# Kernel optimization log

Hardware: AMD Instinct MI355X
Metric: run time of the kernel (lower is better)

Reference implementation:

```python
import jax, jax.numpy as jnp
import numpy as np

LOGIT_SCALE = 1.0 / 0.07  # from ClipLoss(temperature=0.07)


def setup_inputs() -> dict:
    key = jax.random.key(0)
    k1, k2 = jax.random.split(key)
    N, D = 16384, 512
    return {
        "image_features": jax.random.normal(k1, (N, D), dtype=jnp.float32),
        "text_features": jax.random.normal(k2, (N, D), dtype=jnp.float32),
    }


def reference(image_features, text_features):
    # logits_per_image[i, j] = scale * <img_i, txt_j>; logits_per_text is its transpose
    logits_per_image = LOGIT_SCALE * (image_features @ text_features.T)  # [N, N]
    logits_per_text = logits_per_image.T
    n = logits_per_image.shape[0]
    labels = jnp.arange(n)
    # cross_entropy(logits, labels) = mean over rows of (logsumexp(row) - row[label])
    def ce(logits):
        logp = jax.nn.log_softmax(logits, axis=-1)
        return -jnp.mean(jnp.take_along_axis(logp, labels[:, None], axis=-1))
    return (ce(logits_per_image) + ce(logits_per_text)) / 2.0
```

## Files before the change

### kernel.cpp

```cpp
#include <hip/hip_runtime.h>
#include <cstdint>
#include <cstddef>
#include <cmath>


#define N_ROWS 16384
#define DIM    512
#define NB     128
#define SCALE  14.285714285714286f
#define CF     20.609929155556625f
#define LN2F   0.6931471805599453f
#define SP     36

typedef __attribute__((ext_vector_type(8))) int   int8v;
typedef __attribute__((ext_vector_type(4))) int   int4v;
typedef __attribute__((ext_vector_type(4))) float floatx4;

#if __has_builtin(__builtin_amdgcn_exp2f)
#define EXP2(x) __builtin_amdgcn_exp2f(x)
#else
#define EXP2(x) exp2f(x)
#endif

__device__ __forceinline__ void async_load16(const void* g, void* l) {
    __builtin_amdgcn_global_load_lds(
        (__attribute__((address_space(1))) void*)(void*)(g),
        (__attribute__((address_space(3))) void*)(l), 16, 0, 0);
}

__device__ __forceinline__ void lse_merge2(float& m, float& s, float om, float os) {
    float nm = fmaxf(m, om);
    s = s * EXP2(m - nm) + os * EXP2(om - nm);
    m = nm;
}

__device__ __forceinline__ int pk_fp8x4(float a, float b, float c, float d) {
    int u = __builtin_amdgcn_cvt_pk_fp8_f32(a, b, 0, false);
    u = __builtin_amdgcn_cvt_pk_fp8_f32(c, d, u, true);
    return u;
}

__global__ void cvt_diag_kernel(const float* __restrict__ a, const float* __restrict__ b,
                                unsigned char* __restrict__ A8, unsigned char* __restrict__ B8,
                                float* __restrict__ diag) {
    const int t  = threadIdx.x;
    const int rl = t & 15, g16 = t >> 4;
    const int row = blockIdx.x * 16 + rl;
    const float4* ai = (const float4*)(a + (size_t)row * DIM + g16 * 32);
    const float4* bi = (const float4*)(b + (size_t)row * DIM + g16 * 32);
    float dot = 0.f;
    int wa[8], wb[8];
#pragma unroll
    for (int j = 0; j < 4; ++j) {
        float4 x0 = ai[2 * j], x1 = ai[2 * j + 1];
        float4 y0 = bi[2 * j], y1 = bi[2 * j + 1];
        dot += x0.x * y0.x + x0.y * y0.y + x0.z * y0.z + x0.w * y0.w
             + x1.x * y1.x + x1.y * y1.y + x1.z * y1.z + x1.w * y1.w;
        wa[2 * j]     = pk_fp8x4(CF * x0.x, CF * x0.y, CF * x0.z, CF * x0.w);
        wa[2 * j + 1] = pk_fp8x4(CF * x1.x, CF * x1.y, CF * x1.z, CF * x1.w);
        wb[2 * j]     = pk_fp8x4(y0.x, y0.y, y0.z, y0.w);
        wb[2 * j + 1] = pk_fp8x4(y1.x, y1.y, y1.z, y1.w);
    }
    const size_t o = ((size_t)g16 * N_ROWS + row) * 32;
    *(int4v*)(A8 + o)      = (int4v){wa[0], wa[1], wa[2], wa[3]};
    *(int4v*)(A8 + o + 16) = (int4v){wa[4], wa[5], wa[6], wa[7]};
    *(int4v*)(B8 + o)      = (int4v){wb[0], wb[1], wb[2], wb[3]};
    *(int4v*)(B8 + o + 16) = (int4v){wb[4], wb[5], wb[6], wb[7]};

    __shared__ float pd[16][17];
    pd[rl][g16] = dot;
    __syncthreads();
    if (t < 16) {
        float s = 0.f;
#pragma unroll
        for (int j = 0; j < 16; ++j) s += pd[t][j];
        diag[blockIdx.x * 16 + t] = SCALE * s;
    }
}

__global__ void gemm_lse_kernel(const unsigned char* __restrict__ A8,
                                const unsigned char* __restrict__ B8,
                                float* __restrict__ row_m, float* __restrict__ row_s,
                                float* __restrict__ col_m, float* __restrict__ col_s) {
    __shared__ __align__(16) unsigned char smem[32768];
    unsigned char* sA = smem;
    unsigned char* sB = smem + 16384;
    float* part = (float*)smem;

    const int t = threadIdx.x;
    const int bid = blockIdx.x;

    const int xcd   = bid & 7;
    const int local = bid >> 3;
    const int br    = xcd * 16 + (local & 15);
    const int bc    = local >> 4;

    const int lane = t & 63;
    const int w    = t >> 6;
    const int quad = lane >> 4;
    const int l15  = lane & 15;
    const int wrow = w >> 1;
    const int wcol = w & 1;

    floatx4 acc[4][4];
#pragma unroll
    for (int i = 0; i < 4; ++i)
#pragma unroll
        for (int j = 0; j < 4; ++j)
            acc[i][j] = (floatx4){0.f, 0.f, 0.f, 0.f};

    const int isB   = w >> 1;
    const int gbase = (w & 1) * 2;
    const unsigned char* gsrc = isB ? B8 : A8;
    const int rbase = (isB ? bc : br) * 128;
    unsigned char* lbase = isB ? sB : sA;

    const unsigned char* gp[8];
    unsigned char* lp[8];
#pragma unroll
    for (int c = 0; c < 8; ++c) {
        const int g = gbase + (c >> 2), i = c & 3;
        gp[c] = gsrc + ((size_t)g * N_ROWS + rbase) * 32 + i * 1024 + lane * 16;
        lp[c] = lbase + g * 4096 + i * 1024;
    }
    const size_t kbstr = (size_t)4 * N_ROWS * 32;

    for (int kb = 0; kb < 4; ++kb) {
        const size_t ko = (size_t)kb * kbstr;
#pragma unroll
        for (int c = 0; c < 8; ++c) async_load16(gp[c] + ko, lp[c]);
        __builtin_amdgcn_s_waitcnt(0);
        __syncthreads();

        int8v av[4], bv[4];
#pragma unroll
        for (int mi = 0; mi < 4; ++mi) {
            const unsigned char* p = sA + (quad * 128 + wrow * 64 + mi * 16 + l15) * 32;
            int4v lo = *(const int4v*)p;
            int4v hi = *(const int4v*)(p + 16);
            av[mi] = (int8v){lo[0], lo[1], lo[2], lo[3], hi[0], hi[1], hi[2], hi[3]};
        }
#pragma unroll
        for (int ni = 0; ni < 4; ++ni) {
            const unsigned char* p = sB + (quad * 128 + wcol * 64 + ni * 16 + l15) * 32;
            int4v lo = *(const int4v*)p;
            int4v hi = *(const int4v*)(p + 16);
            bv[ni] = (int8v){lo[0], lo[1], lo[2], lo[3], hi[0], hi[1], hi[2], hi[3]};
        }
#pragma unroll
        for (int mi = 0; mi < 4; ++mi)
#pragma unroll
            for (int ni = 0; ni < 4; ++ni)
                acc[mi][ni] = __builtin_amdgcn_mfma_scale_f32_16x16x128_f8f6f4(
                    av[mi], bv[ni], acc[mi][ni], 0, 0, 0, 127, 0, 127);
        __syncthreads();
    }


#pragma unroll
    for (int mi = 0; mi < 4; ++mi)
#pragma unroll
        for (int r = 0; r < 4; ++r) {
            float pm = fmaxf(fmaxf(acc[mi][0][r], acc[mi][1][r]),
                             fmaxf(acc[mi][2][r], acc[mi][3][r]));
            int lrow = wrow * 64 + mi * 16 + quad * 4 + r;
            part[lrow * SP + wcol * 16 + l15] = pm;
        }

#pragma unroll
    for (int ni = 0; ni < 4; ++ni) {
        float m = acc[0][ni][0];
#pragma unroll
        for (int mi = 0; mi < 4; ++mi)
#pragma unroll
            for (int r = 0; r < 4; ++r)
                m = fmaxf(m, acc[mi][ni][r]);
        m = fmaxf(m, __shfl_xor(m, 16));
        m = fmaxf(m, __shfl_xor(m, 32));
        float s = 0.f;
#pragma unroll
        for (int mi = 0; mi < 4; ++mi)
#pragma unroll
            for (int r = 0; r < 4; ++r)
                s += EXP2(acc[mi][ni][r] - m);
        s += __shfl_xor(s, 16);
        s += __shfl_xor(s, 32);
        if (quad == 0) {
            int cl = wcol * 64 + ni * 16 + l15;
            part[cl * SP + 32 + wrow] = m;
            part[cl * SP + 34 + wrow] = s;
        }
    }
    __syncthreads();

    if (t < 128) {
        float m = part[t * SP + 32], s = part[t * SP + 34];
        lse_merge2(m, s, part[t * SP + 33], part[t * SP + 35]);
        col_m[(size_t)br * N_ROWS + bc * 128 + t] = m;
        col_s[(size_t)br * N_ROWS + bc * 128 + t] = s;
        const float4* p4 = (const float4*)&part[t * SP];
        float4 v = p4[0];
#pragma unroll
        for (int j = 1; j < 8; ++j) {
            float4 u = p4[j];
            v.x = fmaxf(v.x, u.x); v.y = fmaxf(v.y, u.y);
            v.z = fmaxf(v.z, u.z); v.w = fmaxf(v.w, u.w);
        }
        part[t * SP + 32] = fmaxf(fmaxf(v.x, v.y), fmaxf(v.z, v.w));
    }
    __syncthreads();

#pragma unroll
    for (int mi = 0; mi < 4; ++mi)
#pragma unroll
        for (int r = 0; r < 4; ++r) {
            int lrow = wrow * 64 + mi * 16 + quad * 4 + r;
            float m = part[lrow * SP + 32];
            float s = EXP2(acc[mi][0][r] - m) + EXP2(acc[mi][1][r] - m)
                    + EXP2(acc[mi][2][r] - m) + EXP2(acc[mi][3][r] - m);
            part[lrow * SP + wcol * 16 + l15] = s;
        }
    __syncthreads();

    if (t < 128) {
        const float4* p4 = (const float4*)&part[t * SP];
        float4 v = p4[0];
#pragma unroll
        for (int j = 1; j < 8; ++j) {
            float4 u = p4[j];
            v.x += u.x; v.y += u.y; v.z += u.z; v.w += u.w;
        }
        float s = (v.x + v.y) + (v.z + v.w);
        float m = part[t * SP + 32];
        row_m[(size_t)bc * N_ROWS + br * 128 + t] = m;
        row_s[(size_t)bc * N_ROWS + br * 128 + t] = s;
    }
}

__global__ void reduce_kernel(const float* __restrict__ row_m, const float* __restrict__ row_s,
                              const float* __restrict__ col_m, const float* __restrict__ col_s,
                              const float* __restrict__ diag, float* __restrict__ out) {
    const int w = threadIdx.x >> 6, lane = threadIdx.x & 63;
    const int row = blockIdx.x * 64 + lane;
    const size_t jt0 = (size_t)w * 32;

    float m = row_m[jt0 * N_ROWS + row];
    float s = row_s[jt0 * N_ROWS + row];
    for (int k = 1; k < 32; ++k)
        lse_merge2(m, s, row_m[(jt0 + k) * N_ROWS + row], row_s[(jt0 + k) * N_ROWS + row]);
    float mc = col_m[jt0 * N_ROWS + row];
    float sc = col_s[jt0 * N_ROWS + row];
    for (int k = 1; k < 32; ++k)
        lse_merge2(mc, sc, col_m[(jt0 + k) * N_ROWS + row], col_s[(jt0 + k) * N_ROWS + row]);

    __shared__ float sm[4][64], ss[4][64], tm[4][64], ts[4][64];
    sm[w][lane] = m;  ss[w][lane] = s;
    tm[w][lane] = mc; ts[w][lane] = sc;
    __syncthreads();

    if (w == 0) {
#pragma unroll
        for (int h = 1; h < 4; ++h) lse_merge2(m, s, sm[h][lane], ss[h][lane]);
        float lse_r = m + log2f(s);
#pragma unroll
        for (int h = 1; h < 4; ++h) lse_merge2(mc, sc, tm[h][lane], ts[h][lane]);
        float lse_c = mc + log2f(sc);
        float contrib = 0.5f * LN2F * (lse_r + lse_c) - diag[row];
        for (int mask = 32; mask; mask >>= 1) contrib += __shfl_xor(contrib, mask);
        if (lane == 0) atomicAdd(out, contrib * (1.0f / N_ROWS));
    }
}

extern "C" void kernel_launch(void* const* d_in, const int* in_sizes, int n_in,
                              void* d_out, int out_size, void* d_ws, size_t ws_size,
                              hipStream_t stream) {
    const float* img = (const float*)d_in[0];
    const float* txt = (const float*)d_in[1];
    char* ws = (char*)d_ws;

    const size_t MB = 1024 * 1024;
    unsigned char* A8 = (unsigned char*)(ws);
    unsigned char* B8 = (unsigned char*)(ws + 8 * MB);
    float* row_m = (float*)(ws + 16 * MB);
    float* row_s = (float*)(ws + 24 * MB);
    float* col_m = (float*)(ws + 32 * MB);
    float* col_s = (float*)(ws + 40 * MB);
    float* diag  = (float*)(ws + 48 * MB);
    float* out   = (float*)d_out;

    hipMemsetAsync(d_out, 0, sizeof(float), stream);
    cvt_diag_kernel<<<N_ROWS / 16, 256, 0, stream>>>(img, txt, A8, B8, diag);
    gemm_lse_kernel<<<NB * NB, 256, 0, stream>>>(A8, B8, row_m, row_s, col_m, col_s);
    reduce_kernel<<<N_ROWS / 64, 256, 0, stream>>>(row_m, row_s, col_m, col_s, diag, out);
}
```

Measured before the change: 321.7 us.

## Enlarge GEMM-LSE tile to 256x128 rows with 512-thread blocks

Doubles the row dimension of each block's output tile to 256 rows using 8 waves, so each block loads a 256-row A strip and a 128-row B strip. The intent is to raise operand reuse and cut global/L2 traffic and the number of partial column LSE records, which also halves the column merge work in the reduce kernel. In exchange it needs 48KB of LDS and larger blocks, which lowers how many blocks fit per CU and adds an extra sync in the epilogue.

```diff
diff --git a/kernel.cpp b/kernel.cpp
--- a/kernel.cpp
+++ b/kernel.cpp
@@ -6,11 +6,12 @@
 
 #define N_ROWS 16384
 #define DIM    512
-#define NB     128
+#define NBR    64
+#define NBC    128
 #define SCALE  14.285714285714286f
 #define CF     20.609929155556625f
 #define LN2F   0.6931471805599453f
-#define SP     36
+#define SP     40
 
 typedef __attribute__((ext_vector_type(8))) int   int8v;
 typedef __attribute__((ext_vector_type(4))) int   int4v;
@@ -78,13 +79,14 @@
     }
 }
 
-__global__ void gemm_lse_kernel(const unsigned char* __restrict__ A8,
-                                const unsigned char* __restrict__ B8,
-                                float* __restrict__ row_m, float* __restrict__ row_s,
-                                float* __restrict__ col_m, float* __restrict__ col_s) {
-    __shared__ __align__(16) unsigned char smem[32768];
+__global__ __launch_bounds__(512)
+void gemm_lse_kernel(const unsigned char* __restrict__ A8,
+                     const unsigned char* __restrict__ B8,
+                     float* __restrict__ row_m, float* __restrict__ row_s,
+                     float* __restrict__ col_m, float* __restrict__ col_s) {
+    __shared__ __align__(16) unsigned char smem[49152];
     unsigned char* sA = smem;
-    unsigned char* sB = smem + 16384;
+    unsigned char* sB = smem + 32768;
     float* part = (float*)smem;
 
     const int t = threadIdx.x;
@@ -92,8 +94,8 @@
 
     const int xcd   = bid & 7;
     const int local = bid >> 3;
-    const int br    = xcd * 16 + (local & 15);
-    const int bc    = local >> 4;
+    const int br    = xcd * 8 + (local & 7);
+    const int bc    = local >> 3;
 
     const int lane = t & 63;
     const int w    = t >> 6;
@@ -109,33 +111,34 @@
         for (int j = 0; j < 4; ++j)
             acc[i][j] = (floatx4){0.f, 0.f, 0.f, 0.f};
 
-    const int isB   = w >> 1;
-    const int gbase = (w & 1) * 2;
-    const unsigned char* gsrc = isB ? B8 : A8;
-    const int rbase = (isB ? bc : br) * 128;
-    unsigned char* lbase = isB ? sB : sA;
-
-    const unsigned char* gp[8];
-    unsigned char* lp[8];
-#pragma unroll
-    for (int c = 0; c < 8; ++c) {
-        const int g = gbase + (c >> 2), i = c & 3;
-        gp[c] = gsrc + ((size_t)g * N_ROWS + rbase) * 32 + i * 1024 + lane * 16;
-        lp[c] = lbase + g * 4096 + i * 1024;
+    const unsigned char* gp[6];
+    unsigned int lofs[6];
+#pragma unroll
+    for (int c = 0; c < 6; ++c) {
+        const int p = c * 8 + w;
+        if (p < 32) {
+            const int g = p >> 3, i = p & 7;
+            gp[c]   = A8 + ((size_t)g * N_ROWS + br * 256 + i * 32) * 32 + lane * 16;
+            lofs[c] = g * 8192u + i * 1024u;
+        } else {
+            const int q = p - 32, g = q >> 2, i = q & 3;
+            gp[c]   = B8 + ((size_t)g * N_ROWS + bc * 128 + i * 32) * 32 + lane * 16;
+            lofs[c] = 32768u + g * 4096u + i * 1024u;
+        }
     }
     const size_t kbstr = (size_t)4 * N_ROWS * 32;
 
     for (int kb = 0; kb < 4; ++kb) {
         const size_t ko = (size_t)kb * kbstr;
 #pragma unroll
-        for (int c = 0; c < 8; ++c) async_load16(gp[c] + ko, lp[c]);
+        for (int c = 0; c < 6; ++c) async_load16(gp[c] + ko, smem + lofs[c]);
         __builtin_amdgcn_s_waitcnt(0);
         __syncthreads();
 
         int8v av[4], bv[4];
 #pragma unroll
         for (int mi = 0; mi < 4; ++mi) {
-            const unsigned char* p = sA + (quad * 128 + wrow * 64 + mi * 16 + l15) * 32;
+            const unsigned char* p = sA + (quad * 256 + wrow * 64 + mi * 16 + l15) * 32;
             int4v lo = *(const int4v*)p;
             int4v hi = *(const int4v*)(p + 16);
             av[mi] = (int8v){lo[0], lo[1], lo[2], lo[3], hi[0], hi[1], hi[2], hi[3]};
@@ -188,16 +191,22 @@
         if (quad == 0) {
             int cl = wcol * 64 + ni * 16 + l15;
             part[cl * SP + 32 + wrow] = m;
-            part[cl * SP + 34 + wrow] = s;
+            part[cl * SP + 36 + wrow] = s;
         }
     }
     __syncthreads();
 
     if (t < 128) {
-        float m = part[t * SP + 32], s = part[t * SP + 34];
-        lse_merge2(m, s, part[t * SP + 33], part[t * SP + 35]);
+        float m = part[t * SP + 32], s = part[t * SP + 36];
+#pragma unroll
+        for (int h = 1; h < 4; ++h)
+            lse_merge2(m, s, part[t * SP + 32 + h], part[t * SP + 36 + h]);
         col_m[(size_t)br * N_ROWS + bc * 128 + t] = m;
         col_s[(size_t)br * N_ROWS + bc * 128 + t] = s;
+    }
+    __syncthreads();
+
+    if (t < 256) {
         const float4* p4 = (const float4*)&part[t * SP];
         float4 v = p4[0];
 #pragma unroll
@@ -222,7 +231,7 @@
         }
     __syncthreads();
 
-    if (t < 128) {
+    if (t < 256) {
         const float4* p4 = (const float4*)&part[t * SP];
         float4 v = p4[0];
 #pragma unroll
@@ -232,8 +241,8 @@
         }
         float s = (v.x + v.y) + (v.z + v.w);
         float m = part[t * SP + 32];
-        row_m[(size_t)bc * N_ROWS + br * 128 + t] = m;
-        row_s[(size_t)bc * N_ROWS + br * 128 + t] = s;
+        row_m[(size_t)bc * N_ROWS + br * 256 + t] = m;
+        row_s[(size_t)bc * N_ROWS + br * 256 + t] = s;
     }
 }
 
@@ -242,16 +251,18 @@
                               const float* __restrict__ diag, float* __restrict__ out) {
     const int w = threadIdx.x >> 6, lane = threadIdx.x & 63;
     const int row = blockIdx.x * 64 + lane;
-    const size_t jt0 = (size_t)w * 32;
-
-    float m = row_m[jt0 * N_ROWS + row];
-    float s = row_s[jt0 * N_ROWS + row];
+
+    const size_t jr0 = (size_t)w * 32;
+    float m = row_m[jr0 * N_ROWS + row];
+    float s = row_s[jr0 * N_ROWS + row];
     for (int k = 1; k < 32; ++k)
-        lse_merge2(m, s, row_m[(jt0 + k) * N_ROWS + row], row_s[(jt0 + k) * N_ROWS + row]);
-    float mc = col_m[jt0 * N_ROWS + row];
-    float sc = col_s[jt0 * N_ROWS + row];
-    for (int k = 1; k < 32; ++k)
-        lse_merge2(mc, sc, col_m[(jt0 + k) * N_ROWS + row], col_s[(jt0 + k) * N_ROWS + row]);
+        lse_merge2(m, s, row_m[(jr0 + k) * N_ROWS + row], row_s[(jr0 + k) * N_ROWS + row]);
+
+    const size_t jc0 = (size_t)w * 16;
+    float mc = col_m[jc0 * N_ROWS + row];
+    float sc = col_s[jc0 * N_ROWS + row];
+    for (int k = 1; k < 16; ++k)
+        lse_merge2(mc, sc, col_m[(jc0 + k) * N_ROWS + row], col_s[(jc0 + k) * N_ROWS + row]);
 
     __shared__ float sm[4][64], ss[4][64], tm[4][64], ts[4][64];
     sm[w][lane] = m;  ss[w][lane] = s;
@@ -290,6 +301,6 @@
 
     hipMemsetAsync(d_out, 0, sizeof(float), stream);
     cvt_diag_kernel<<<N_ROWS / 16, 256, 0, stream>>>(img, txt, A8, B8, diag);
-    gemm_lse_kernel<<<NB * NB, 256, 0, stream>>>(A8, B8, row_m, row_s, col_m, col_s);
+    gemm_lse_kernel<<<NBR * NBC, 512, 0, stream>>>(A8, B8, row_m, row_s, col_m, col_s);
     reduce_kernel<<<N_ROWS / 64, 256, 0, stream>>>(row_m, row_s, col_m, col_s, diag, out);
 }
```

After: 410.1 us. +27.5%, slower.

## Load FP8 GEMM fragments directly from global memory, bypassing LDS staging

Applied to the files above, without the earlier changes.

Removes the global-to-LDS async staging and the per-k-block barriers in the GEMM+LSE kernel. Each wave now reads its A and B MFMA fragments straight from global memory, relying on the pre-swizzled layout and L2 for reuse. The LDS buffer shrinks to just the reduction scratch, and launch bounds are set to allow 4 blocks per CU. The trade-off is redundant global/L2 traffic, since each fragment is read by two waves, and load latency that is no longer overlapped by an explicit staging step.

```diff
diff --git a/kernel.cpp b/kernel.cpp
--- a/kernel.cpp
+++ b/kernel.cpp
@@ -22,12 +22,6 @@
 #define EXP2(x) exp2f(x)
 #endif
 
-__device__ __forceinline__ void async_load16(const void* g, void* l) {
-    __builtin_amdgcn_global_load_lds(
-        (__attribute__((address_space(1))) void*)(void*)(g),
-        (__attribute__((address_space(3))) void*)(l), 16, 0, 0);
-}
-
 __device__ __forceinline__ void lse_merge2(float& m, float& s, float om, float os) {
     float nm = fmaxf(m, om);
     s = s * EXP2(m - nm) + os * EXP2(om - nm);
@@ -38,6 +32,10 @@
     int u = __builtin_amdgcn_cvt_pk_fp8_f32(a, b, 0, false);
     u = __builtin_amdgcn_cvt_pk_fp8_f32(c, d, u, true);
     return u;
+}
+
+__device__ __forceinline__ int8v frag8(int4v lo, int4v hi) {
+    return (int8v){lo[0], lo[1], lo[2], lo[3], hi[0], hi[1], hi[2], hi[3]};
 }
 
 __global__ void cvt_diag_kernel(const float* __restrict__ a, const float* __restrict__ b,
@@ -78,14 +76,12 @@
     }
 }
 
-__global__ void gemm_lse_kernel(const unsigned char* __restrict__ A8,
-                                const unsigned char* __restrict__ B8,
-                                float* __restrict__ row_m, float* __restrict__ row_s,
-                                float* __restrict__ col_m, float* __restrict__ col_s) {
-    __shared__ __align__(16) unsigned char smem[32768];
-    unsigned char* sA = smem;
-    unsigned char* sB = smem + 16384;
-    float* part = (float*)smem;
+__global__ __launch_bounds__(256, 4)
+void gemm_lse_kernel(const unsigned char* __restrict__ A8,
+                     const unsigned char* __restrict__ B8,
+                     float* __restrict__ row_m, float* __restrict__ row_s,
+                     float* __restrict__ col_m, float* __restrict__ col_s) {
+    __shared__ __align__(16) float part[NB * SP];
 
     const int t = threadIdx.x;
     const int bid = blockIdx.x;
@@ -109,51 +105,32 @@
         for (int j = 0; j < 4; ++j)
             acc[i][j] = (floatx4){0.f, 0.f, 0.f, 0.f};
 
-    const int isB   = w >> 1;
-    const int gbase = (w & 1) * 2;
-    const unsigned char* gsrc = isB ? B8 : A8;
-    const int rbase = (isB ? bc : br) * 128;
-    unsigned char* lbase = isB ? sB : sA;
-
-    const unsigned char* gp[8];
-    unsigned char* lp[8];
-#pragma unroll
-    for (int c = 0; c < 8; ++c) {
-        const int g = gbase + (c >> 2), i = c & 3;
-        gp[c] = gsrc + ((size_t)g * N_ROWS + rbase) * 32 + i * 1024 + lane * 16;
-        lp[c] = lbase + g * 4096 + i * 1024;
-    }
-    const size_t kbstr = (size_t)4 * N_ROWS * 32;
-
+    unsigned int offA = ((unsigned)quad * N_ROWS
+                         + (unsigned)(br * 128 + wrow * 64 + l15)) * 32u;
+    unsigned int offB = ((unsigned)quad * N_ROWS
+                         + (unsigned)(bc * 128 + wcol * 64 + l15)) * 32u;
+    const unsigned int kstep = 4u * N_ROWS * 32u;
+
+#pragma unroll
     for (int kb = 0; kb < 4; ++kb) {
-        const size_t ko = (size_t)kb * kbstr;
-#pragma unroll
-        for (int c = 0; c < 8; ++c) async_load16(gp[c] + ko, lp[c]);
-        __builtin_amdgcn_s_waitcnt(0);
-        __syncthreads();
-
-        int8v av[4], bv[4];
+        int4v alo[4], ahi[4];
 #pragma unroll
         for (int mi = 0; mi < 4; ++mi) {
-            const unsigned char* p = sA + (quad * 128 + wrow * 64 + mi * 16 + l15) * 32;
-            int4v lo = *(const int4v*)p;
-            int4v hi = *(const int4v*)(p + 16);
-            av[mi] = (int8v){lo[0], lo[1], lo[2], lo[3], hi[0], hi[1], hi[2], hi[3]};
+            alo[mi] = *(const int4v*)(A8 + offA + mi * 512);
+            ahi[mi] = *(const int4v*)(A8 + offA + mi * 512 + 16);
         }
 #pragma unroll
         for (int ni = 0; ni < 4; ++ni) {
-            const unsigned char* p = sB + (quad * 128 + wcol * 64 + ni * 16 + l15) * 32;
-            int4v lo = *(const int4v*)p;
-            int4v hi = *(const int4v*)(p + 16);
-            bv[ni] = (int8v){lo[0], lo[1], lo[2], lo[3], hi[0], hi[1], hi[2], hi[3]};
-        }
-#pragma unroll
-        for (int mi = 0; mi < 4; ++mi)
-#pragma unroll
-            for (int ni = 0; ni < 4; ++ni)
+            int4v bl = *(const int4v*)(B8 + offB + ni * 512);
+            int4v bh = *(const int4v*)(B8 + offB + ni * 512 + 16);
+            int8v bv = frag8(bl, bh);
+#pragma unroll
+            for (int mi = 0; mi < 4; ++mi)
                 acc[mi][ni] = __builtin_amdgcn_mfma_scale_f32_16x16x128_f8f6f4(
-                    av[mi], bv[ni], acc[mi][ni], 0, 0, 0, 127, 0, 127);
-        __syncthreads();
+                    frag8(alo[mi], ahi[mi]), bv, acc[mi][ni], 0, 0, 0, 127, 0, 127);
+        }
+        offA += kstep;
+        offB += kstep;
     }
 
 
```

New measurement: 292.2 us. 1.1x faster.
